# Kernel tuning notes

Measured on AMD Instinct MI355X. Metric: run time of the kernel, lower is better.

## Reference

```python
import jax, jax.numpy as jnp
import numpy as np
import math

B, D, E = 32768, 256, 8          # batch, feature dim (shape=[256]), num_steps experts
T_TOTAL = 1.0
H_STEP = T_TOTAL / E             # self.h
EIGMIN, EIGINIT, EIGMAX = -1.0, 0.0, 1.0
LOGIT_099 = math.log(0.99 / 0.01)


def setup_inputs() -> dict:
    key = jax.random.key(0)
    k_t, k_y, k_w1, k_w2 = jax.random.split(key, 4)
    std = 1.0 / math.sqrt(D)     # xavier-ish init for expert weights
    return {
        "t": jax.random.uniform(k_t, (B,), dtype=jnp.float32),            # times in [0, T)
        "y": jax.random.normal(k_y, (B, D), dtype=jnp.float32),
        "W1": jax.random.normal(k_w1, (E, D, D), dtype=jnp.float32) * std,
        "b1": jnp.zeros((E, D), dtype=jnp.float32),
        "W2": jax.random.normal(k_w2, (E, D, D), dtype=jnp.float32) * std,
        "b2": jnp.zeros((E, D), dtype=jnp.float32),
        "scales": jnp.full((1, D), LOGIT_099, dtype=jnp.float32),         # learn_scales=False init
        "shifta": jnp.asarray(LOGIT_099, dtype=jnp.float32),
        "shiftb": jnp.asarray(LOGIT_099, dtype=jnp.float32),
    }


def reference(t, y, W1, b1, W2, b2, scales, shifta, shiftb):
    # t2ind: clamp(int(t / h), max=E-1)
    ind = jnp.minimum((t / H_STEP).astype(jnp.int32), E - 1)            # [B]
    # per-sample dispatch to expert F[i] (2-layer MLP), grouped as masked
    # dense batched GEMMs per expert (E is a small fixed set)
    f = jnp.zeros_like(y)
    for e in range(E):
        h_e = jnp.tanh(jnp.einsum('bd,kd->bk', y, W1[e]) + b1[e])       # [B, D]
        f_e = jnp.einsum('bd,kd->bk', h_e, W2[e]) + b2[e]               # [B, D]
        f = jnp.where((ind == e)[:, None], f_e, f)
    # sigmoid-scale / affine-combine epilogue
    f = jax.nn.sigmoid(scales) * f
    a = EIGINIT + jax.nn.sigmoid(shifta) * (EIGMIN - EIGINIT)
    b = EIGINIT + jax.nn.sigmoid(shiftb) * (EIGMAX - EIGINIT)
    return 0.5 * ((b - a) * f + (a + b) * y)
```

## Files before the change

kernel.cpp:

```cpp
#include <hip/hip_runtime.h>

#define BATCH 32768
#define DIM   256
#define NEXP  8
#define MT    32
#define STRIDE 264

typedef __bf16 bf16x8 __attribute__((ext_vector_type(8)));
typedef __bf16 bf16x4 __attribute__((ext_vector_type(4)));
typedef float  f32x16 __attribute__((ext_vector_type(16)));

static __device__ __forceinline__ float sigmoid_f(float x) {
    return __builtin_amdgcn_rcpf(1.f + __expf(-x));
}
static __device__ __forceinline__ float tanh_f(float x) {
    return 1.f - 2.f * __builtin_amdgcn_rcpf(__expf(2.f * x) + 1.f);
}

static __device__ __forceinline__ void lds_barrier() {
    asm volatile("s_waitcnt lgkmcnt(0)\n\ts_barrier" ::: "memory");
}

__global__ void prep_kernel(const float* __restrict__ W1, const float* __restrict__ W2,
                            const float* __restrict__ t,
                            bf16x8* __restrict__ W1p, bf16x8* __restrict__ W2p,
                            int* __restrict__ cursor, int* __restrict__ idxb) {
    const int b = blockIdx.x;
    if (b < 256) {
        const int tid = b * 256 + threadIdx.x;
        const int kh  = tid & 1;
        const int ks  = (tid >> 1) & 15;
        const int col = (tid >> 5) & 255;
        const int e   = tid >> 13;
        const long src = (long)tid * 8;
        const float4 a0 = *(const float4*)(W1 + src);
        const float4 a1 = *(const float4*)(W1 + src + 4);
        const float4 c0 = *(const float4*)(W2 + src);
        const float4 c1 = *(const float4*)(W2 + src + 4);
        bf16x8 w1, w2;
        w1[0] = (__bf16)a0.x; w1[1] = (__bf16)a0.y; w1[2] = (__bf16)a0.z; w1[3] = (__bf16)a0.w;
        w1[4] = (__bf16)a1.x; w1[5] = (__bf16)a1.y; w1[6] = (__bf16)a1.z; w1[7] = (__bf16)a1.w;
        w2[0] = (__bf16)c0.x; w2[1] = (__bf16)c0.y; w2[2] = (__bf16)c0.z; w2[3] = (__bf16)c0.w;
        w2[4] = (__bf16)c1.x; w2[5] = (__bf16)c1.y; w2[6] = (__bf16)c1.z; w2[7] = (__bf16)c1.w;
        const int dst = (e << 13) | ((col >> 5) << 10) | (ks << 6) | (kh << 5) | (col & 31);
        W1p[dst] = w1;
        W2p[dst] = w2;
    } else {
        __shared__ int h[NEXP], base[NEXP];
        if (threadIdx.x < NEXP) h[threadIdx.x] = 0;
        __syncthreads();
        const int i = (b - 256) * 256 + threadIdx.x;
        const int e = min((int)(t[i] * 8.0f), NEXP - 1);
        const int lr = atomicAdd(&h[e], 1);
        __syncthreads();
        if (threadIdx.x < NEXP)
            base[threadIdx.x] = atomicAdd(&cursor[threadIdx.x], h[threadIdx.x]);
        __syncthreads();
        idxb[e * BATCH + base[e] + lr] = i;
    }
}

__global__ void __launch_bounds__(512, 2)
mlp_kernel(const float* __restrict__ y,
           const float* __restrict__ scales,
           const float* __restrict__ shifta,
           const float* __restrict__ shiftb,
           const float* __restrict__ b1,
           const float* __restrict__ b2,
           const bf16x8* __restrict__ W1p,
           const bf16x8* __restrict__ W2p,
           const int* __restrict__ cnt,
           const int* __restrict__ idxb,
           float* __restrict__ out) {
    __shared__ __bf16 ab[MT * STRIDE];
    __shared__ int rows[MT];

    const int tx   = threadIdx.x;
    const int wave = tx >> 6;
    const int lane = tx & 63;
    const int nl   = lane & 31;
    const int kh   = lane >> 5;
    const int n    = wave * 32 + nl;

    const int e    = blockIdx.x >> 5;
    const int slot = blockIdx.x & 31;
    const int ce   = cnt[e];
    const int nt_e = (ce + MT - 1) >> 5;
    if (slot >= nt_e) return;
    const int* idx_e = idxb + e * BATCH;

    const bf16x8* w1p = W1p + (e << 13) + (wave << 10) + lane;
    const bf16x8* w2p = W2p + (e << 13) + (wave << 10) + lane;
    bf16x8 wA[16], wB[16];
#pragma unroll
    for (int ks = 0; ks < 16; ++ks) {
        wA[ks] = w1p[ks << 6];
        wB[ks] = w2p[ks << 6];
    }

    const float sa = sigmoid_f(shifta[0]);
    const float sb = sigmoid_f(shiftb[0]);
    const float k1 = 0.5f * (sb + sa);
    const float k2 = 0.5f * (sb - sa);
    const bool needy = (k2 != 0.0f);
    const float c1  = k1 * sigmoid_f(scales[n]);
    const float b1v = b1[(e << 8) | n];
    const float b2v = b2[(e << 8) | n];

    int ti = slot;
    int nrows = min(MT, ce - ti * MT);
    {
        const int rbase = ti * MT;
#pragma unroll
        for (int p = 0; p < 4; ++p) {
            const int r  = p * 8 + wave;
            const int rr = min(r, nrows - 1);
            const int g  = idx_e[rbase + rr];
            if (lane == 0) rows[r] = (r < nrows) ? g : -1;
            const float4 v = *(const float4*)(y + (long)g * DIM + lane * 4);
            bf16x4 w;
            w[0] = (__bf16)v.x; w[1] = (__bf16)v.y; w[2] = (__bf16)v.z; w[3] = (__bf16)v.w;
            *(bf16x4*)(ab + r * STRIDE + lane * 4) = w;
        }
    }
    lds_barrier();

    for (;;) {
        const int ti2 = ti + 32;
        const bool have_next = (ti2 < nt_e);
        int nrows2 = 0;
        int g2v[4];
        float4 v2[4];
        if (have_next) {
            nrows2 = min(MT, ce - ti2 * MT);
            const int rbase2 = ti2 * MT;
#pragma unroll
            for (int p = 0; p < 4; ++p) {
                const int r  = p * 8 + wave;
                const int rr = min(r, nrows2 - 1);
                g2v[p] = idx_e[rbase2 + rr];
            }
#pragma unroll
            for (int p = 0; p < 4; ++p)
                v2[p] = *(const float4*)(y + (long)g2v[p] * DIM + lane * 4);
        }

        const __bf16* apt0 = ab + nl * STRIDE + kh * 8;

        f32x16 acc = {};
#pragma unroll
        for (int ks = 0; ks < 16; ++ks) {
            bf16x8 a0 = *(const bf16x8*)(apt0 + ks * 16);
            acc = __builtin_amdgcn_mfma_f32_32x32x16_bf16(a0, wA[ks], acc, 0, 0, 0);
        }
        lds_barrier();

#pragma unroll
        for (int r = 0; r < 16; ++r) {
            const int row = (r & 3) + ((r >> 2) << 3) + (kh << 2);
            ab[row * STRIDE + n] = (__bf16)tanh_f(acc[r] + b1v);
        }
        lds_barrier();

        f32x16 acc2 = {};
#pragma unroll
        for (int ks = 0; ks < 16; ++ks) {
            bf16x8 a0 = *(const bf16x8*)(apt0 + ks * 16);
            acc2 = __builtin_amdgcn_mfma_f32_32x32x16_bf16(a0, wB[ks], acc2, 0, 0, 0);
        }

#pragma unroll
        for (int r = 0; r < 16; ++r) {
            const int row = (r & 3) + ((r >> 2) << 3) + (kh << 2);
            const int g = rows[row];
            if (g >= 0) {
                float res = c1 * (acc2[r] + b2v);
                if (needy) res += k2 * y[(long)g * DIM + n];
                out[(long)g * DIM + n] = res;
            }
        }

        if (!have_next) return;

        lds_barrier();

#pragma unroll
        for (int p = 0; p < 4; ++p) {
            const int r = p * 8 + wave;
            if (lane == 0) rows[r] = (r < nrows2) ? g2v[p] : -1;
            const float4 v = v2[p];
            bf16x4 w;
            w[0] = (__bf16)v.x; w[1] = (__bf16)v.y; w[2] = (__bf16)v.z; w[3] = (__bf16)v.w;
            *(bf16x4*)(ab + r * STRIDE + lane * 4) = w;
        }
        lds_barrier();

        ti = ti2; nrows = nrows2;
    }
}

extern "C" void kernel_launch(void* const* d_in, const int* in_sizes, int n_in,
                              void* d_out, int out_size, void* d_ws, size_t ws_size,
                              hipStream_t stream) {
    const float* t      = (const float*)d_in[0];
    const float* y      = (const float*)d_in[1];
    const float* W1     = (const float*)d_in[2];
    const float* b1     = (const float*)d_in[3];
    const float* W2     = (const float*)d_in[4];
    const float* b2     = (const float*)d_in[5];
    const float* scales = (const float*)d_in[6];
    const float* shifta = (const float*)d_in[7];
    const float* shiftb = (const float*)d_in[8];
    float* out = (float*)d_out;

    char* ws = (char*)d_ws;
    int* cursor = (int*)ws;
    int* idxb   = (int*)(ws + 256);
    bf16x8* W1p = (bf16x8*)(ws + 256 + NEXP * BATCH * 4);
    bf16x8* W2p = W1p + 65536;

    hipMemsetAsync(cursor, 0, 32, stream);
    prep_kernel<<<384, 256, 0, stream>>>(W1, W2, t, W1p, W2p, cursor, idxb);
    mlp_kernel<<<256, 512, 0, stream>>>(y, scales, shifta, shiftb, b1, b2,
                                        W1p, W2p, cursor, idxb, out);
}
```

Before: 127.0 us.

## Warp-specialize MLP kernel: split GEMM1 and GEMM2 waves with double-buffered pipeline

Splits the eight waves into two groups: the first computes the hidden layer (GEMM1 plus tanh) into a double-buffered LDS tile, the second computes GEMM2, writes output and stages the next input tile. Tiles flow through a two-stage software pipeline with a single barrier per step instead of several. This is meant to overlap the two GEMMs and the gather loads across tiles, at the cost of doubled LDS usage and an extra pipeline fill/drain step per block.

```diff
diff --git a/kernel.cpp b/kernel.cpp
--- a/kernel.cpp
+++ b/kernel.cpp
@@ -72,130 +72,138 @@
            const int* __restrict__ cnt,
            const int* __restrict__ idxb,
            float* __restrict__ out) {
-    __shared__ __bf16 ab[MT * STRIDE];
-    __shared__ int rows[MT];
+    __shared__ __bf16 Y[2][MT * STRIDE];
+    __shared__ __bf16 H[2][MT * STRIDE];
+    __shared__ int rowsb[4][MT];
 
     const int tx   = threadIdx.x;
     const int wave = tx >> 6;
     const int lane = tx & 63;
     const int nl   = lane & 31;
     const int kh   = lane >> 5;
-    const int n    = wave * 32 + nl;
+    const bool isG1 = (wave < 4);
+    const int  w    = wave & 3;
+    const int  n0   = w * 64 + nl;
+    const int  n1   = n0 + 32;
 
     const int e    = blockIdx.x >> 5;
     const int slot = blockIdx.x & 31;
     const int ce   = cnt[e];
     const int nt_e = (ce + MT - 1) >> 5;
     if (slot >= nt_e) return;
+    const int nt   = ((nt_e - slot) + 31) >> 5;
     const int* idx_e = idxb + e * BATCH;
 
-    const bf16x8* w1p = W1p + (e << 13) + (wave << 10) + lane;
-    const bf16x8* w2p = W2p + (e << 13) + (wave << 10) + lane;
-    bf16x8 wA[16], wB[16];
-#pragma unroll
-    for (int ks = 0; ks < 16; ++ks) {
-        wA[ks] = w1p[ks << 6];
-        wB[ks] = w2p[ks << 6];
-    }
+    const bf16x8* wp = (isG1 ? W1p : W2p) + (e << 13) + ((w * 2) << 10) + lane;
+    bf16x8 wf[2][16];
+#pragma unroll
+    for (int s = 0; s < 2; ++s)
+#pragma unroll
+        for (int ks = 0; ks < 16; ++ks)
+            wf[s][ks] = wp[(s << 10) + (ks << 6)];
 
     const float sa = sigmoid_f(shifta[0]);
     const float sb = sigmoid_f(shiftb[0]);
     const float k1 = 0.5f * (sb + sa);
     const float k2 = 0.5f * (sb - sa);
     const bool needy = (k2 != 0.0f);
-    const float c1  = k1 * sigmoid_f(scales[n]);
-    const float b1v = b1[(e << 8) | n];
-    const float b2v = b2[(e << 8) | n];
-
-    int ti = slot;
-    int nrows = min(MT, ce - ti * MT);
-    {
-        const int rbase = ti * MT;
-#pragma unroll
-        for (int p = 0; p < 4; ++p) {
-            const int r  = p * 8 + wave;
-            const int rr = min(r, nrows - 1);
+    float b1v[2], b2v[2], cc[2];
+    b1v[0] = b1[(e << 8) | n0]; b1v[1] = b1[(e << 8) | n1];
+    b2v[0] = b2[(e << 8) | n0]; b2v[1] = b2[(e << 8) | n1];
+    cc[0]  = k1 * sigmoid_f(scales[n0]); cc[1] = k1 * sigmoid_f(scales[n1]);
+
+    if (!isG1) {
+        const int rbase = slot * MT;
+        const int nr = min(MT, ce - rbase);
+#pragma unroll
+        for (int p = 0; p < 8; ++p) {
+            const int r  = w * 8 + p;
+            const int rr = min(r, nr - 1);
             const int g  = idx_e[rbase + rr];
-            if (lane == 0) rows[r] = (r < nrows) ? g : -1;
+            if (lane == 0) rowsb[0][r] = (r < nr) ? g : -1;
             const float4 v = *(const float4*)(y + (long)g * DIM + lane * 4);
-            bf16x4 w;
-            w[0] = (__bf16)v.x; w[1] = (__bf16)v.y; w[2] = (__bf16)v.z; w[3] = (__bf16)v.w;
-            *(bf16x4*)(ab + r * STRIDE + lane * 4) = w;
+            bf16x4 wv;
+            wv[0] = (__bf16)v.x; wv[1] = (__bf16)v.y; wv[2] = (__bf16)v.z; wv[3] = (__bf16)v.w;
+            *(bf16x4*)(&Y[0][r * STRIDE + lane * 4]) = wv;
         }
     }
     lds_barrier();
 
-    for (;;) {
-        const int ti2 = ti + 32;
-        const bool have_next = (ti2 < nt_e);
-        int nrows2 = 0;
-        int g2v[4];
-        float4 v2[4];
-        if (have_next) {
-            nrows2 = min(MT, ce - ti2 * MT);
-            const int rbase2 = ti2 * MT;
-#pragma unroll
-            for (int p = 0; p < 4; ++p) {
-                const int r  = p * 8 + wave;
-                const int rr = min(r, nrows2 - 1);
-                g2v[p] = idx_e[rbase2 + rr];
-            }
-#pragma unroll
-            for (int p = 0; p < 4; ++p)
-                v2[p] = *(const float4*)(y + (long)g2v[p] * DIM + lane * 4);
-        }
-
-        const __bf16* apt0 = ab + nl * STRIDE + kh * 8;
-
-        f32x16 acc = {};
-#pragma unroll
-        for (int ks = 0; ks < 16; ++ks) {
-            bf16x8 a0 = *(const bf16x8*)(apt0 + ks * 16);
-            acc = __builtin_amdgcn_mfma_f32_32x32x16_bf16(a0, wA[ks], acc, 0, 0, 0);
+    for (int t = 0; t <= nt; ++t) {
+        if (isG1) {
+            if (t < nt) {
+                const __bf16* ap = &Y[t & 1][nl * STRIDE + kh * 8];
+                f32x16 a0v = {}, a1v = {};
+#pragma unroll
+                for (int ks = 0; ks < 16; ++ks) {
+                    bf16x8 a = *(const bf16x8*)(ap + ks * 16);
+                    a0v = __builtin_amdgcn_mfma_f32_32x32x16_bf16(a, wf[0][ks], a0v, 0, 0, 0);
+                    a1v = __builtin_amdgcn_mfma_f32_32x32x16_bf16(a, wf[1][ks], a1v, 0, 0, 0);
+                }
+                __bf16* hb = &H[t & 1][0];
+#pragma unroll
+                for (int r = 0; r < 16; ++r) {
+                    const int row = (r & 3) + ((r >> 2) << 3) + (kh << 2);
+                    hb[row * STRIDE + n0] = (__bf16)tanh_f(a0v[r] + b1v[0]);
+                    hb[row * STRIDE + n1] = (__bf16)tanh_f(a1v[r] + b1v[1]);
+                }
+            }
+        } else {
+            const bool do_stage = (t + 1 < nt);
+            int gs[8]; float4 vs[8]; int nr2 = 0;
+            if (do_stage) {
+                const int rbase = (slot + (t + 1) * 32) * MT;
+                nr2 = min(MT, ce - rbase);
+#pragma unroll
+                for (int p = 0; p < 8; ++p) {
+                    const int r  = w * 8 + p;
+                    const int rr = min(r, nr2 - 1);
+                    gs[p] = idx_e[rbase + rr];
+                }
+#pragma unroll
+                for (int p = 0; p < 8; ++p)
+                    vs[p] = *(const float4*)(y + (long)gs[p] * DIM + lane * 4);
+            }
+            if (t >= 1) {
+                const __bf16* ap = &H[(t - 1) & 1][nl * STRIDE + kh * 8];
+                f32x16 a0v = {}, a1v = {};
+#pragma unroll
+                for (int ks = 0; ks < 16; ++ks) {
+                    bf16x8 a = *(const bf16x8*)(ap + ks * 16);
+                    a0v = __builtin_amdgcn_mfma_f32_32x32x16_bf16(a, wf[0][ks], a0v, 0, 0, 0);
+                    a1v = __builtin_amdgcn_mfma_f32_32x32x16_bf16(a, wf[1][ks], a1v, 0, 0, 0);
+                }
+                const int* rb = rowsb[(t - 1) & 3];
+#pragma unroll
+                for (int r = 0; r < 16; ++r) {
+                    const int row = (r & 3) + ((r >> 2) << 3) + (kh << 2);
+                    const int g = rb[row];
+                    if (g >= 0) {
+                        float r0 = cc[0] * (a0v[r] + b2v[0]);
+                        float r1 = cc[1] * (a1v[r] + b2v[1]);
+                        if (needy) {
+                            r0 += k2 * y[(long)g * DIM + n0];
+                            r1 += k2 * y[(long)g * DIM + n1];
+                        }
+                        out[(long)g * DIM + n0] = r0;
+                        out[(long)g * DIM + n1] = r1;
+                    }
+                }
+            }
+            if (do_stage) {
+                const int kb = t + 1;
+#pragma unroll
+                for (int p = 0; p < 8; ++p) {
+                    const int r = w * 8 + p;
+                    if (lane == 0) rowsb[kb & 3][r] = (r < nr2) ? gs[p] : -1;
+                    const float4 v = vs[p];
+                    bf16x4 wv;
+                    wv[0] = (__bf16)v.x; wv[1] = (__bf16)v.y; wv[2] = (__bf16)v.z; wv[3] = (__bf16)v.w;
+                    *(bf16x4*)(&Y[kb & 1][r * STRIDE + lane * 4]) = wv;
+                }
+            }
         }
         lds_barrier();
-
-#pragma unroll
-        for (int r = 0; r < 16; ++r) {
-            const int row = (r & 3) + ((r >> 2) << 3) + (kh << 2);
-            ab[row * STRIDE + n] = (__bf16)tanh_f(acc[r] + b1v);
-        }
-        lds_barrier();
-
-        f32x16 acc2 = {};
-#pragma unroll
-        for (int ks = 0; ks < 16; ++ks) {
-            bf16x8 a0 = *(const bf16x8*)(apt0 + ks * 16);
-            acc2 = __builtin_amdgcn_mfma_f32_32x32x16_bf16(a0, wB[ks], acc2, 0, 0, 0);
-        }
-
-#pragma unroll
-        for (int r = 0; r < 16; ++r) {
-            const int row = (r & 3) + ((r >> 2) << 3) + (kh << 2);
-            const int g = rows[row];
-            if (g >= 0) {
-                float res = c1 * (acc2[r] + b2v);
-                if (needy) res += k2 * y[(long)g * DIM + n];
-                out[(long)g * DIM + n] = res;
-            }
-        }
-
-        if (!have_next) return;
-
-        lds_barrier();
-
-#pragma unroll
-        for (int p = 0; p < 4; ++p) {
-            const int r = p * 8 + wave;
-            if (lane == 0) rows[r] = (r < nrows2) ? g2v[p] : -1;
-            const float4 v = v2[p];
-            bf16x4 w;
-            w[0] = (__bf16)v.x; w[1] = (__bf16)v.y; w[2] = (__bf16)v.z; w[3] = (__bf16)v.w;
-            *(bf16x4*)(ab + r * STRIDE + lane * 4) = w;
-        }
-        lds_barrier();
-
-        ti = ti2; nrows = nrows2;
     }
 }
 
```

After: 122.6 us. -3.5%, faster.

## Pre-gather y into per-expert bf16 buffer and double the MLP row tile

Applied to the files above, without the earlier changes.

Adds a separate gather kernel that copies each expert's rows of y, converted to bf16, into a contiguous padded buffer. The MLP kernel then streams contiguous bf16 rows instead of doing an indexed fp32 gather, and it processes 64-row tiles with two MFMA accumulators per wave. The intent is to cut the scattered-load latency and conversion work inside the MLP loop and to reuse each weight register load across more rows. The cost is an extra kernel launch plus a write and re-read of a bf16 copy of y. The residual y term in the epilogue now comes from bf16 rather than fp32, which loses some precision.

```diff
diff --git a/kernel.cpp b/kernel.cpp
--- a/kernel.cpp
+++ b/kernel.cpp
@@ -3,7 +3,7 @@
 #define BATCH 32768
 #define DIM   256
 #define NEXP  8
-#define MT    32
+#define MT    64
 #define STRIDE 264
 
 typedef __bf16 bf16x8 __attribute__((ext_vector_type(8)));
@@ -60,8 +60,32 @@
     }
 }
 
+__global__ void __launch_bounds__(256, 8)
+gather_kernel(const float* __restrict__ y, const int* __restrict__ cnt,
+              const int* __restrict__ idxb, __bf16* __restrict__ yp) {
+    const int wave = threadIdx.x >> 6;
+    const int lane = threadIdx.x & 63;
+    const int wid  = blockIdx.x * 4 + wave;
+    const int totw = gridDim.x * 4;
+#pragma unroll
+    for (int e = 0; e < NEXP; ++e) {
+        const int ce = cnt[e];
+        const int Re = ((ce + 63) >> 6) << 6;
+        const int* idx_e = idxb + e * BATCH;
+        __bf16* yp_e = yp + (long)e * BATCH * DIM;
+        for (int q = wid; q < Re; q += totw) {
+            const int g = idx_e[min(q, ce - 1)];
+            const float4 v = *(const float4*)(y + (long)g * DIM + lane * 4);
+            bf16x4 wv;
+            wv[0] = (__bf16)v.x; wv[1] = (__bf16)v.y;
+            wv[2] = (__bf16)v.z; wv[3] = (__bf16)v.w;
+            *(bf16x4*)(yp_e + (long)q * DIM + lane * 4) = wv;
+        }
+    }
+}
+
 __global__ void __launch_bounds__(512, 2)
-mlp_kernel(const float* __restrict__ y,
+mlp_kernel(const __bf16* __restrict__ yp,
            const float* __restrict__ scales,
            const float* __restrict__ shifta,
            const float* __restrict__ shiftb,
@@ -85,9 +109,10 @@
     const int e    = blockIdx.x >> 5;
     const int slot = blockIdx.x & 31;
     const int ce   = cnt[e];
-    const int nt_e = (ce + MT - 1) >> 5;
-    if (slot >= nt_e) return;
+    const int nt   = (ce + MT - 1) >> 6;
+    if (slot >= nt) return;
     const int* idx_e = idxb + e * BATCH;
+    const __bf16* yp_e = yp + (long)e * BATCH * DIM;
 
     const bf16x8* w1p = W1p + (e << 13) + (wave << 10) + lane;
     const bf16x8* w2p = W2p + (e << 13) + (wave << 10) + lane;
@@ -108,94 +133,86 @@
     const float b2v = b2[(e << 8) | n];
 
     int ti = slot;
-    int nrows = min(MT, ce - ti * MT);
     {
         const int rbase = ti * MT;
-#pragma unroll
-        for (int p = 0; p < 4; ++p) {
-            const int r  = p * 8 + wave;
-            const int rr = min(r, nrows - 1);
-            const int g  = idx_e[rbase + rr];
-            if (lane == 0) rows[r] = (r < nrows) ? g : -1;
-            const float4 v = *(const float4*)(y + (long)g * DIM + lane * 4);
-            bf16x4 w;
-            w[0] = (__bf16)v.x; w[1] = (__bf16)v.y; w[2] = (__bf16)v.z; w[3] = (__bf16)v.w;
-            *(bf16x4*)(ab + r * STRIDE + lane * 4) = w;
+        if (wave == 0) rows[lane] = (lane < ce - rbase) ? idx_e[rbase + lane] : -1;
+#pragma unroll
+        for (int p = 0; p < 8; ++p) {
+            const int r = p * 8 + wave;
+            bf16x4 v = *(const bf16x4*)(yp_e + (long)(rbase + r) * DIM + lane * 4);
+            *(bf16x4*)(ab + r * STRIDE + lane * 4) = v;
         }
     }
     lds_barrier();
 
     for (;;) {
         const int ti2 = ti + 32;
-        const bool have_next = (ti2 < nt_e);
-        int nrows2 = 0;
-        int g2v[4];
-        float4 v2[4];
+        const bool have_next = (ti2 < nt);
+        bf16x4 v2[8];
+        int row2 = -1;
         if (have_next) {
-            nrows2 = min(MT, ce - ti2 * MT);
             const int rbase2 = ti2 * MT;
 #pragma unroll
-            for (int p = 0; p < 4; ++p) {
-                const int r  = p * 8 + wave;
-                const int rr = min(r, nrows2 - 1);
-                g2v[p] = idx_e[rbase2 + rr];
-            }
-#pragma unroll
-            for (int p = 0; p < 4; ++p)
-                v2[p] = *(const float4*)(y + (long)g2v[p] * DIM + lane * 4);
+            for (int p = 0; p < 8; ++p)
+                v2[p] = *(const bf16x4*)(yp_e + (long)(rbase2 + p * 8 + wave) * DIM + lane * 4);
+            if (wave == 0 && lane < ce - rbase2) row2 = idx_e[rbase2 + lane];
         }
 
         const __bf16* apt0 = ab + nl * STRIDE + kh * 8;
-
-        f32x16 acc = {};
+        const __bf16* apt1 = ab + (32 + nl) * STRIDE + kh * 8;
+
+        f32x16 acc[2] = {};
 #pragma unroll
         for (int ks = 0; ks < 16; ++ks) {
             bf16x8 a0 = *(const bf16x8*)(apt0 + ks * 16);
-            acc = __builtin_amdgcn_mfma_f32_32x32x16_bf16(a0, wA[ks], acc, 0, 0, 0);
-        }
-        lds_barrier();
-
-#pragma unroll
-        for (int r = 0; r < 16; ++r) {
-            const int row = (r & 3) + ((r >> 2) << 3) + (kh << 2);
-            ab[row * STRIDE + n] = (__bf16)tanh_f(acc[r] + b1v);
-        }
-        lds_barrier();
-
-        f32x16 acc2 = {};
+            bf16x8 a1 = *(const bf16x8*)(apt1 + ks * 16);
+            acc[0] = __builtin_amdgcn_mfma_f32_32x32x16_bf16(a0, wA[ks], acc[0], 0, 0, 0);
+            acc[1] = __builtin_amdgcn_mfma_f32_32x32x16_bf16(a1, wA[ks], acc[1], 0, 0, 0);
+        }
+        lds_barrier();
+
+#pragma unroll
+        for (int mi = 0; mi < 2; ++mi)
+#pragma unroll
+            for (int r = 0; r < 16; ++r) {
+                const int row = mi * 32 + (r & 3) + ((r >> 2) << 3) + (kh << 2);
+                ab[row * STRIDE + n] = (__bf16)tanh_f(acc[mi][r] + b1v);
+            }
+        lds_barrier();
+
+        f32x16 acc2[2] = {};
 #pragma unroll
         for (int ks = 0; ks < 16; ++ks) {
             bf16x8 a0 = *(const bf16x8*)(apt0 + ks * 16);
-            acc2 = __builtin_amdgcn_mfma_f32_32x32x16_bf16(a0, wB[ks], acc2, 0, 0, 0);
-        }
-
-#pragma unroll
-        for (int r = 0; r < 16; ++r) {
-            const int row = (r & 3) + ((r >> 2) << 3) + (kh << 2);
-            const int g = rows[row];
-            if (g >= 0) {
-                float res = c1 * (acc2[r] + b2v);
-                if (needy) res += k2 * y[(long)g * DIM + n];
-                out[(long)g * DIM + n] = res;
+            bf16x8 a1 = *(const bf16x8*)(apt1 + ks * 16);
+            acc2[0] = __builtin_amdgcn_mfma_f32_32x32x16_bf16(a0, wB[ks], acc2[0], 0, 0, 0);
+            acc2[1] = __builtin_amdgcn_mfma_f32_32x32x16_bf16(a1, wB[ks], acc2[1], 0, 0, 0);
+        }
+
+#pragma unroll
+        for (int mi = 0; mi < 2; ++mi)
+#pragma unroll
+            for (int r = 0; r < 16; ++r) {
+                const int row = mi * 32 + (r & 3) + ((r >> 2) << 3) + (kh << 2);
+                const int g = rows[row];
+                if (g >= 0) {
+                    float res = c1 * (acc2[mi][r] + b2v);
+                    if (needy) res += k2 * (float)yp_e[(long)(ti * MT + row) * DIM + n];
+                    out[(long)g * DIM + n] = res;
+                }
             }
-        }
 
         if (!have_next) return;
 
         lds_barrier();
 
-#pragma unroll
-        for (int p = 0; p < 4; ++p) {
-            const int r = p * 8 + wave;
-            if (lane == 0) rows[r] = (r < nrows2) ? g2v[p] : -1;
-            const float4 v = v2[p];
-            bf16x4 w;
-            w[0] = (__bf16)v.x; w[1] = (__bf16)v.y; w[2] = (__bf16)v.z; w[3] = (__bf16)v.w;
-            *(bf16x4*)(ab + r * STRIDE + lane * 4) = w;
-        }
-        lds_barrier();
-
-        ti = ti2; nrows = nrows2;
+        if (wave == 0) rows[lane] = row2;
+#pragma unroll
+        for (int p = 0; p < 8; ++p)
+            *(bf16x4*)(ab + (p * 8 + wave) * STRIDE + lane * 4) = v2[p];
+        lds_barrier();
+
+        ti = ti2;
     }
 }
 
@@ -218,9 +235,11 @@
     int* idxb   = (int*)(ws + 256);
     bf16x8* W1p = (bf16x8*)(ws + 256 + NEXP * BATCH * 4);
     bf16x8* W2p = W1p + 65536;
+    __bf16* yp  = (__bf16*)(ws + 256 + NEXP * BATCH * 4 + 2 * 1048576);
 
     hipMemsetAsync(cursor, 0, 32, stream);
     prep_kernel<<<384, 256, 0, stream>>>(W1, W2, t, W1p, W2p, cursor, idxb);
-    mlp_kernel<<<256, 512, 0, stream>>>(y, scales, shifta, shiftb, b1, b2,
+    gather_kernel<<<2048, 256, 0, stream>>>(y, cursor, idxb, yp);
+    mlp_kernel<<<256, 512, 0, stream>>>(yp, scales, shifta, shiftb, b1, b2,
                                         W1p, W2p, cursor, idxb, out);
 }
```

Result: slower. 137.9 us (+8.6%).
